# Kernel tuning notes

Measured on AMD Instinct MI355X. Metric: run time of the kernel, lower is better.

Reference implementation:

```python
import jax, jax.numpy as jnp
import numpy as np

N = 131072   # nodes
E = 2097152  # edges (avg degree 16)
B = 4096     # subgraph (center) nodes, ntype == -1
D = 64       # feature dim (in_nfeats == all latent dims)
L = 3        # number of (local, global) RelGraphConv pairs
R = 3        # num relations
NB = 2       # num bases


def setup_inputs() -> dict:
    key = jax.random.key(0)
    ks = jax.random.split(key, 20)
    s = 0.05
    return {
        "x": jax.random.normal(ks[0], (N, D), jnp.float32),
        "src": jax.random.randint(ks[1], (E,), 0, N, jnp.int32),
        "dst": jax.random.randint(ks[2], (E,), 0, N, jnp.int32),
        "etype": jax.random.randint(ks[3], (E,), 0, R, jnp.int32),
        "mask": jax.random.uniform(ks[4], (E,), jnp.float32),
        "mask2": jax.random.uniform(ks[5], (E,), jnp.float32),
        # local RelGraphConv params (basis decomposition): W_r = sum_b C[r,b] * V[b]
        "lV": jax.random.normal(ks[6], (L, NB, D, D), jnp.float32) * s,
        "lC": jax.random.normal(ks[7], (L, R, NB), jnp.float32),
        "lW": jax.random.normal(ks[8], (L, D, D), jnp.float32) * s,   # self-loop weight
        "lB": jnp.zeros((L, D), jnp.float32),
        # global RelGraphConv params
        "gV": jax.random.normal(ks[9], (L, NB, D, D), jnp.float32) * s,
        "gC": jax.random.normal(ks[10], (L, R, NB), jnp.float32),
        "gW": jax.random.normal(ks[11], (L, D, D), jnp.float32) * s,
        "gB": jnp.zeros((L, D), jnp.float32),
        # MLP head: lin1 (sum(latent_dim)=192 -> 128), lin2 (128 -> 1)
        "w1": jax.random.normal(ks[12], (128, L * D), jnp.float32) * s,
        "b1": jnp.zeros((128,), jnp.float32),
        "w2": jax.random.normal(ks[13], (1, 128), jnp.float32) * s,
        "b2": jnp.zeros((1,), jnp.float32),
        "num_subg": B,
    }


def _rel_graph_conv(h, V, C, W, b, src, dst, etype, norm):
    """Basis-decomposed RelGraphConv with self-loop (DGL semantics, eval mode)."""
    n = h.shape[0]
    hV = jnp.einsum('nd,bdo->nbo', h, V)                  # [N, NB, D]
    coef = C[etype]                                        # [E, NB] edge-type gather
    msg = jnp.einsum('eb,ebo->eo', coef, hV[src])          # [E, D]
    msg = msg * norm[:, None]                              # per-edge norm (edge_mask)
    agg = jax.ops.segment_sum(msg, dst, num_segments=n)    # scatter-add to dst
    return agg + h @ W + b                                 # + self-loop + bias


def reference(x, src, dst, etype, mask, mask2, lV, lC, lW, lB,
              gV, gC, gW, gB, w1, b1, w2, b2, num_subg):
    # eval mode: edge_drop and Dropout(0.5) are identity
    h = x
    subg_states = []
    for i in range(L):
        h = jax.nn.elu(_rel_graph_conv(h, lV[i], lC[i], lW[i], lB[i],
                                       src, dst, etype, mask))
        # (ui_states collected in original but unused for 'center' embedding)
        h = jax.nn.leaky_relu(_rel_graph_conv(h, gV[i], gC[i], gW[i], gB[i],
                                              src, dst, etype, mask2),
                              negative_slope=0.01)
        subg_states.append(h)
    subg = jnp.concatenate(subg_states, axis=1)[:num_subg]  # subgraph-center nodes
    hid = jnp.maximum(subg @ w1.T + b1, 0.0)
    out = jax.nn.sigmoid(hid @ w2.T + b2)
    return out[:, 0]
```

## Files before the change

kernel.cpp:

```cpp
#include <hip/hip_runtime.h>
#include <math.h>

#define N_NODES 131072
#define N_EDGES 2097152
#define DIM     64
#define BSUB    4096
#define NREL    3
#define NBASES  2
#define NCB     256
#define CBSZ    8192

typedef unsigned short u16;
typedef __attribute__((ext_vector_type(8))) short bf16x8;
typedef __attribute__((ext_vector_type(4))) float f32x4;

__device__ __forceinline__ float bf2f(u16 x) {
    return __uint_as_float(((unsigned)x) << 16);
}
__device__ __forceinline__ u16 f2bf(float f) {
    unsigned u = __float_as_uint(f);
    unsigned r = (u + 0x7FFFu + ((u >> 16) & 1u)) >> 16;
    return (u16)r;
}
__device__ __forceinline__ float4 bf4_to_f4(ushort4 u) {
    return make_float4(bf2f(u.x), bf2f(u.y), bf2f(u.z), bf2f(u.w));
}
__device__ __forceinline__ ushort4 f4_to_bf4(float4 v) {
    ushort4 o; o.x = f2bf(v.x); o.y = f2bf(v.y); o.z = f2bf(v.z); o.w = f2bf(v.w);
    return o;
}


__global__ void initmark_kernel(int* __restrict__ mark, int* __restrict__ chist) {
    int i = blockIdx.x * 256 + threadIdx.x;
    if (i < N_NODES) mark[i] = (i < BSUB) ? 1 : 0;
    if (i < NCB) chist[i] = 0;
}

__global__ __launch_bounds__(256) void chist_kernel(const int* __restrict__ dst,
                                                    int* __restrict__ chist) {
    __shared__ int lh[NCB];
    int tid = threadIdx.x;
    lh[tid] = 0;
    __syncthreads();
    int base = blockIdx.x * CBSZ + tid;
#pragma unroll
    for (int j = 0; j < CBSZ / 256; j++)
        atomicAdd(&lh[dst[base + j * 256] >> 9], 1);
    __syncthreads();
    atomicAdd(&chist[tid], lh[tid]);
}

__global__ void cscan_kernel(const int* __restrict__ chist, int* __restrict__ cbase,
                             int* __restrict__ ccur, int* __restrict__ offs) {
    __shared__ int s[NCB];
    int tid = threadIdx.x;
    int v = chist[tid];
    s[tid] = v;
    __syncthreads();
    int val = v;
    for (int off = 1; off < NCB; off <<= 1) {
        int tmp = (tid >= off) ? s[tid - off] : 0;
        __syncthreads();
        val += tmp;
        s[tid] = val;
        __syncthreads();
    }
    cbase[tid] = val - v;
    ccur[tid] = val - v;
    if (tid == 0) offs[N_NODES] = N_EDGES;
}

__global__ __launch_bounds__(256) void cscatter_kernel(
    const int* __restrict__ src, const int* __restrict__ dst,
    const int* __restrict__ et, const float* __restrict__ m1,
    const float* __restrict__ m2, int* __restrict__ ccur,
    int4* __restrict__ tmp, int* __restrict__ mark) {
    __shared__ int lh[NCB];
    __shared__ int lbase[NCB];
    int tid = threadIdx.x;
    lh[tid] = 0;
    __syncthreads();
    int e0 = blockIdx.x * CBSZ;
#pragma unroll
    for (int j = 0; j < CBSZ / 256; j++)
        atomicAdd(&lh[dst[e0 + tid + j * 256] >> 9], 1);
    __syncthreads();
    int c = lh[tid];
    lbase[tid] = c ? atomicAdd(&ccur[tid], c) : 0;
    lh[tid] = 0;
    __syncthreads();
#pragma unroll
    for (int j = 0; j < CBSZ / 256; j++) {
        int e = e0 + tid + j * 256;
        int d = dst[e];
        int s = src[e];
        int b = d >> 9;
        int r = atomicAdd(&lh[b], 1);
        int4 v;
        v.x = s | (et[e] << 20);
        v.y = __float_as_int(m1[e]);
        v.z = __float_as_int(m2[e]);
        v.w = d;
        tmp[lbase[b] + r] = v;
        if (d < BSUB) mark[s] = 1;
    }
}

__global__ __launch_bounds__(256) void fscatter_kernel(
    const int4* __restrict__ tmp, const int* __restrict__ cbase,
    const int* __restrict__ chist, int* __restrict__ offs,
    int4* __restrict__ csr) {
    __shared__ int lh[512];
    __shared__ int lpre[512];
    __shared__ int s2[256];
    int b = blockIdx.x;
    int tid = threadIdx.x;
    int base = cbase[b], cnt = chist[b];
    lh[tid] = 0; lh[tid + 256] = 0;
    __syncthreads();
    for (int i = tid; i < cnt; i += 256)
        atomicAdd(&lh[tmp[base + i].w & 511], 1);
    __syncthreads();
    int a0 = lh[2 * tid], a1 = lh[2 * tid + 1];
    s2[tid] = a0 + a1;
    __syncthreads();
    int val = s2[tid];
    for (int off = 1; off < 256; off <<= 1) {
        int t = (tid >= off) ? s2[tid - off] : 0;
        __syncthreads();
        val += t;
        s2[tid] = val;
        __syncthreads();
    }
    int ex = val - (a0 + a1);
    lpre[2 * tid] = ex;
    lpre[2 * tid + 1] = ex + a0;
    offs[b * 512 + 2 * tid]     = base + ex;
    offs[b * 512 + 2 * tid + 1] = base + ex + a0;
    lh[tid] = 0; lh[tid + 256] = 0;
    __syncthreads();
    for (int i = tid; i < cnt; i += 256) {
        int4 v = tmp[base + i];
        int k = v.w & 511;
        int r = atomicAdd(&lh[k], 1);
        csr[base + lpre[k] + r] = v;
    }
}

__global__ void scan1_kernel(const int* __restrict__ cnt, int* __restrict__ scanned,
                             int* __restrict__ bsum) {
    __shared__ int s[256];
    int tid = threadIdx.x;
    int i = blockIdx.x * 256 + tid;
    int v = cnt[i];
    s[tid] = v;
    __syncthreads();
    int val = v;
    for (int off = 1; off < 256; off <<= 1) {
        int tmp = (tid >= off) ? s[tid - off] : 0;
        __syncthreads();
        val += tmp;
        s[tid] = val;
        __syncthreads();
    }
    scanned[i] = val - v;
    if (tid == 255) bsum[blockIdx.x] = val;
}

__global__ void scan2_kernel(int* __restrict__ bsum) {
    __shared__ int s[512];
    int tid = threadIdx.x;
    int v = bsum[tid];
    s[tid] = v;
    __syncthreads();
    int val = v;
    for (int off = 1; off < 512; off <<= 1) {
        int tmp = (tid >= off) ? s[tid - off] : 0;
        __syncthreads();
        val += tmp;
        s[tid] = val;
        __syncthreads();
    }
    bsum[tid] = val - v;
}

__global__ void listfill_kernel(const int* __restrict__ mark, const int* __restrict__ mpref,
                                const int* __restrict__ mbsum, int* __restrict__ list,
                                int* __restrict__ nld) {
    int i = blockIdx.x * 256 + threadIdx.x;
    int pos = mpref[i] + mbsum[blockIdx.x];
    if (mark[i]) list[pos] = i;
    if (i == N_NODES - 1) *nld = pos + mark[i];
}

__global__ void cvt_kernel(const float4* __restrict__ x, ushort4* __restrict__ hb, int n4) {
    int i = blockIdx.x * 256 + threadIdx.x;
    if (i < n4) hb[i] = f4_to_bf4(x[i]);
}

__global__ void wpack_kernel(const float* __restrict__ lV, const float* __restrict__ lW,
                             const float* __restrict__ gV, const float* __restrict__ gW,
                             u16* __restrict__ wfrag) {
    int idx = blockIdx.x * 256 + threadIdx.x;
    if (idx >= 6 * 4 * 6 * 64) return;
    int lane = idx & 63;
    int kidx = (idx >> 6) % 6;
    int nt   = (idx >> 6) / 6 % 4;
    int c    = idx / (64 * 6 * 4);
    int layer = c >> 1;
    bool isglobal = c & 1;
    const float* V = isglobal ? gV : lV;
    const float* W = isglobal ? gW : lW;
    int n = nt * 16 + (lane & 15);
    int kbase = kidx * 32 + (lane >> 4) * 8;
    u16 vals[8];
#pragma unroll
    for (int j = 0; j < 8; j++) {
        int r = kbase + j;
        float val;
        if (r < NBASES * DIM) {
            int b = r >> 6, d = r & 63;
            val = V[((layer * NBASES + b) * DIM + d) * DIM + n];
        } else {
            int d = r - NBASES * DIM;
            val = W[(layer * DIM + d) * DIM + n];
        }
        vals[j] = f2bf(val);
    }
    ushort4* o = (ushort4*)(wfrag + (size_t)idx * 8);
    o[0] = make_ushort4(vals[0], vals[1], vals[2], vals[3]);
    o[1] = make_ushort4(vals[4], vals[5], vals[6], vals[7]);
}

__global__ __launch_bounds__(256) void agg_kernel(
    const ushort4* __restrict__ hb, const int* __restrict__ offs,
    const int4* __restrict__ csr, const float* __restrict__ Cc,
    int which, ushort4* __restrict__ t, int nNodes,
    const int* __restrict__ list, const int* __restrict__ nld) {
    __shared__ int4 lmeta[4][64];
    int lane = threadIdx.x & 63;
    int wid  = threadIdx.x >> 6;
    int idx = (blockIdx.x << 2) + wid;
    int n;
    if (list) {
        if (idx >= *nld) return;
        n = list[idx];
    } else {
        if (idx >= nNodes) return;
        n = idx;
    }
    int q  = lane >> 4;
    int ql = lane & 15;
    float Ca0 = Cc[0], Cb0 = Cc[1], Ca1 = Cc[2], Cb1 = Cc[3], Ca2 = Cc[4], Cb2 = Cc[5];
    int beg = offs[n], end = offs[n + 1];
    float4 a0 = make_float4(0.f, 0.f, 0.f, 0.f);
    float4 a1 = make_float4(0.f, 0.f, 0.f, 0.f);
    for (int base = beg; base < end; base += 64) {
        int cnt = min(64, end - base);
        int pp = 0; float c0 = 0.f, c1 = 0.f;
        if (lane < cnt) {
            int4 meta = csr[base + lane];
            int et = ((unsigned)meta.x) >> 20;
            float m = __int_as_float(which ? meta.z : meta.y);
            float ca = et == 0 ? Ca0 : (et == 1 ? Ca1 : Ca2);
            float cb = et == 0 ? Cb0 : (et == 1 ? Cb1 : Cb2);
            pp = (meta.x & 0xFFFFF) << 4;
            c0 = m * ca;
            c1 = m * cb;
        }
        lmeta[wid][lane] = make_int4(pp, __float_as_int(c0), __float_as_int(c1), 0);
        for (int j = 0; j < cnt; j += 16) {
#pragma unroll
            for (int s = 0; s < 4; s++) {
                int4 md = lmeta[wid][j + (s << 2) + q];
                ushort4 rv = hb[md.x + ql];
                float4 v = bf4_to_f4(rv);
                float e0 = __int_as_float(md.y);
                float e1 = __int_as_float(md.z);
                a0.x = fmaf(e0, v.x, a0.x); a0.y = fmaf(e0, v.y, a0.y);
                a0.z = fmaf(e0, v.z, a0.z); a0.w = fmaf(e0, v.w, a0.w);
                a1.x = fmaf(e1, v.x, a1.x); a1.y = fmaf(e1, v.y, a1.y);
                a1.z = fmaf(e1, v.z, a1.z); a1.w = fmaf(e1, v.w, a1.w);
            }
        }
    }
#pragma unroll
    for (int off = 16; off < 64; off <<= 1) {
        a0.x += __shfl_xor(a0.x, off, 64); a0.y += __shfl_xor(a0.y, off, 64);
        a0.z += __shfl_xor(a0.z, off, 64); a0.w += __shfl_xor(a0.w, off, 64);
        a1.x += __shfl_xor(a1.x, off, 64); a1.y += __shfl_xor(a1.y, off, 64);
        a1.z += __shfl_xor(a1.z, off, 64); a1.w += __shfl_xor(a1.w, off, 64);
    }
    ushort4 outv = f4_to_bf4(q == 0 ? a0 : a1);
    if (q < 2)
        t[(size_t)n * 32 + (q << 4) + ql] = outv;
}

__global__ __launch_bounds__(256) void gemm_kernel(
    const u16* __restrict__ t, const u16* __restrict__ h,
    const u16* __restrict__ wfrag, const float* __restrict__ bias,
    u16* __restrict__ hout, float* __restrict__ subg, int subg_off, int act,
    const int* __restrict__ list, const int* __restrict__ nld) {
    int tid = threadIdx.x;
    int wave = tid >> 6, lane = tid & 63;
    int l16 = lane & 15, quad = lane >> 4;
    int nL = list ? *nld : 0;
    if (list && blockIdx.x * 64 >= nL) return;
    int slot0 = blockIdx.x * 64 + wave * 16;
    int myslot = slot0 + l16;
    int rowA = list ? list[min(myslot, nL - 1)] : myslot;
    const u16* trow = t + (size_t)rowA * 128;
    const u16* hrow = h + (size_t)rowA * 64;
    f32x4 acc0 = {0.f, 0.f, 0.f, 0.f};
    f32x4 acc1 = {0.f, 0.f, 0.f, 0.f};
    f32x4 acc2 = {0.f, 0.f, 0.f, 0.f};
    f32x4 acc3 = {0.f, 0.f, 0.f, 0.f};
#pragma unroll
    for (int kidx = 0; kidx < 6; kidx++) {
        bf16x8 a = (kidx < 4)
            ? *(const bf16x8*)(trow + kidx * 32 + quad * 8)
            : *(const bf16x8*)(hrow + (kidx - 4) * 32 + quad * 8);
        bf16x8 b0 = *(const bf16x8*)(wfrag + ((size_t)(0 * 6 + kidx) * 64 + lane) * 8);
        bf16x8 b1 = *(const bf16x8*)(wfrag + ((size_t)(1 * 6 + kidx) * 64 + lane) * 8);
        bf16x8 b2 = *(const bf16x8*)(wfrag + ((size_t)(2 * 6 + kidx) * 64 + lane) * 8);
        bf16x8 b3 = *(const bf16x8*)(wfrag + ((size_t)(3 * 6 + kidx) * 64 + lane) * 8);
        acc0 = __builtin_amdgcn_mfma_f32_16x16x32_bf16(a, b0, acc0, 0, 0, 0);
        acc1 = __builtin_amdgcn_mfma_f32_16x16x32_bf16(a, b1, acc1, 0, 0, 0);
        acc2 = __builtin_amdgcn_mfma_f32_16x16x32_bf16(a, b2, acc2, 0, 0, 0);
        acc3 = __builtin_amdgcn_mfma_f32_16x16x32_bf16(a, b3, acc3, 0, 0, 0);
    }
    float accs[4][4] = {
        {acc0[0], acc0[1], acc0[2], acc0[3]},
        {acc1[0], acc1[1], acc1[2], acc1[3]},
        {acc2[0], acc2[1], acc2[2], acc2[3]},
        {acc3[0], acc3[1], acc3[2], acc3[3]},
    };
#pragma unroll
    for (int nt = 0; nt < 4; nt++) {
        int col = nt * 16 + l16;
        float bcol = bias[col];
#pragma unroll
        for (int r = 0; r < 4; r++) {
            int cslot = slot0 + quad * 4 + r;
            if (list && cslot >= nL) continue;
            int row = list ? __shfl(rowA, quad * 4 + r, 64) : cslot;
            float xv = accs[nt][r] + bcol;
            float v = act ? (xv > 0.f ? xv : 0.01f * xv)
                          : (xv > 0.f ? xv : expm1f(xv));
            hout[(size_t)row * 64 + col] = f2bf(v);
            if (subg && row < BSUB)
                subg[(size_t)row * 192 + subg_off + col] = v;
        }
    }
}

__global__ __launch_bounds__(256) void head_kernel(
    const float* __restrict__ subg, const float* __restrict__ w1,
    const float* __restrict__ b1, const float* __restrict__ w2,
    const float* __restrict__ b2, float* __restrict__ out) {
    __shared__ float srow[4][192];
    int lane = threadIdx.x & 63, wid = threadIdx.x >> 6;
    int row = blockIdx.x * 4 + wid;
    const float* sr = subg + (size_t)row * 192;
    srow[wid][lane] = sr[lane];
    srow[wid][64 + lane] = sr[64 + lane];
    srow[wid][128 + lane] = sr[128 + lane];
    __syncthreads();
    float acc1 = b1[lane], acc2 = b1[64 + lane];
    const float* w1a = w1 + lane * 192;
    const float* w1b = w1 + (64 + lane) * 192;
    for (int k = 0; k < 192; k++) {
        float s = srow[wid][k];
        acc1 = fmaf(s, w1a[k], acc1);
        acc2 = fmaf(s, w1b[k], acc2);
    }
    acc1 = fmaxf(acc1, 0.f);
    acc2 = fmaxf(acc2, 0.f);
    float part = acc1 * w2[lane] + acc2 * w2[64 + lane];
    for (int off = 32; off; off >>= 1) part += __shfl_down(part, off, 64);
    if (lane == 0) out[row] = 1.f / (1.f + expf(-(part + b2[0])));
}

extern "C" void kernel_launch(void* const* d_in, const int* in_sizes, int n_in,
                              void* d_out, int out_size, void* d_ws, size_t ws_size,
                              hipStream_t stream) {
    const float* x     = (const float*)d_in[0];
    const int*   src   = (const int*)d_in[1];
    const int*   dst   = (const int*)d_in[2];
    const int*   etype = (const int*)d_in[3];
    const float* mask  = (const float*)d_in[4];
    const float* mask2 = (const float*)d_in[5];
    const float* lV = (const float*)d_in[6];
    const float* lC = (const float*)d_in[7];
    const float* lW = (const float*)d_in[8];
    const float* lB = (const float*)d_in[9];
    const float* gV = (const float*)d_in[10];
    const float* gC = (const float*)d_in[11];
    const float* gW = (const float*)d_in[12];
    const float* gB = (const float*)d_in[13];
    const float* w1 = (const float*)d_in[14];
    const float* b1 = (const float*)d_in[15];
    const float* w2 = (const float*)d_in[16];
    const float* b2 = (const float*)d_in[17];
    float* out = (float*)d_out;

    char* ws = (char*)d_ws;
    size_t off = 0;
    auto alloc = [&](size_t bytes) {
        void* p = ws + off;
        off += (bytes + 255) & ~(size_t)255;
        return p;
    };
    ushort4* h    = (ushort4*)alloc((size_t)N_NODES * 64 * 2);
    ushort4* t    = (ushort4*)alloc((size_t)N_NODES * 128 * 2);
    int4*  csr    = (int4*)alloc((size_t)N_EDGES * 16);
    int*   offs   = (int*)alloc((size_t)(N_NODES + 1) * 4);
    int*   chist  = (int*)alloc(NCB * 4);
    int*   cbase  = (int*)alloc(NCB * 4);
    int*   ccur   = (int*)alloc(NCB * 4);
    int*   bsum   = (int*)alloc(512 * 4);
    int*   mark   = (int*)alloc((size_t)N_NODES * 4);
    int*   mpref  = (int*)alloc((size_t)N_NODES * 4);
    int*   mbsum  = (int*)alloc(512 * 4);
    int*   list   = (int*)alloc((size_t)N_NODES * 4);
    int*   nld    = (int*)alloc(256);
    u16*   wfrag  = (u16*)alloc((size_t)6 * 4 * 6 * 64 * 8 * 2);
    float* subg   = (float*)alloc((size_t)BSUB * 192 * 4);
    int4*  tmp    = (int4*)t;

    initmark_kernel<<<N_NODES / 256, 256, 0, stream>>>(mark, chist);
    chist_kernel<<<NCB, 256, 0, stream>>>(dst, chist);
    cscan_kernel<<<1, NCB, 0, stream>>>(chist, cbase, ccur, offs);
    cscatter_kernel<<<NCB, 256, 0, stream>>>(src, dst, etype, mask, mask2,
                                             ccur, tmp, mark);
    fscatter_kernel<<<NCB, 256, 0, stream>>>(tmp, cbase, chist, offs, csr);
    scan1_kernel<<<N_NODES / 256, 256, 0, stream>>>(mark, mpref, mbsum);
    scan2_kernel<<<1, 512, 0, stream>>>(mbsum);
    listfill_kernel<<<N_NODES / 256, 256, 0, stream>>>(mark, mpref, mbsum, list, nld);
    wpack_kernel<<<(6 * 4 * 6 * 64 + 255) / 256, 256, 0, stream>>>(lV, lW, gV, gW, wfrag);
    cvt_kernel<<<(N_NODES * 64 / 4) / 256, 256, 0, stream>>>((const float4*)x, h,
                                                             N_NODES * 64 / 4);

    const int convfrag = 4 * 6 * 64 * 8;
    for (int layer = 0; layer < 3; layer++) {
        const int* ll  = (layer == 2) ? list : nullptr;
        agg_kernel<<<N_NODES / 4, 256, 0, stream>>>(h, offs, csr,
            lC + layer * NREL * NBASES, 0, t, N_NODES, ll, nld);
        gemm_kernel<<<N_NODES / 64, 256, 0, stream>>>(
            (const u16*)t, (const u16*)h,
            wfrag + (size_t)(layer * 2 + 0) * convfrag, lB + layer * 64,
            (u16*)h, nullptr, 0, 0, ll, nld);
        int nG = (layer == 2) ? BSUB : N_NODES;
        agg_kernel<<<(nG + 3) / 4, 256, 0, stream>>>(h, offs, csr,
            gC + layer * NREL * NBASES, 1, t, nG, nullptr, nld);
        gemm_kernel<<<nG / 64, 256, 0, stream>>>(
            (const u16*)t, (const u16*)h,
            wfrag + (size_t)(layer * 2 + 1) * convfrag, gB + layer * 64,
            (u16*)h, subg, layer * 64, 1, nullptr, nld);
    }
    head_kernel<<<BSUB / 4, 256, 0, stream>>>(subg, w1, b1, w2, b2, out);
}
```

Before: 622.2 us.

## Use 512 coarse buckets and vectorize edge loads in CSR build kernels

The coarse dst bucketing for the CSR build goes from 256 buckets of 512 nodes to 512 buckets of 256 nodes. The fine scatter therefore runs 512 blocks, each with 256-entry histograms and a single-element-per-thread scan. The histogram, coarse scatter and fine scatter kernels now read edges as int4 vectors, with four items per thread. The goal is more parallelism and fewer load instructions in the preprocessing phase, at the cost of more global atomics on the coarse cursor and a launch geometry that depends on exact divisibility and alignment.

Result: faster. 603.3 us (-3.0%).

```diff
diff --git a/kernel.cpp b/kernel.cpp
--- a/kernel.cpp
+++ b/kernel.cpp
@@ -7,7 +7,7 @@
 #define BSUB    4096
 #define NREL    3
 #define NBASES  2
-#define NCB     256
+#define NCB     512
 #define CBSZ    8192
 
 typedef unsigned short u16;
@@ -41,14 +41,20 @@
                                                     int* __restrict__ chist) {
     __shared__ int lh[NCB];
     int tid = threadIdx.x;
-    lh[tid] = 0;
-    __syncthreads();
-    int base = blockIdx.x * CBSZ + tid;
-#pragma unroll
-    for (int j = 0; j < CBSZ / 256; j++)
-        atomicAdd(&lh[dst[base + j * 256] >> 9], 1);
+    lh[tid] = 0; lh[tid + 256] = 0;
+    __syncthreads();
+    int base = blockIdx.x * CBSZ;
+#pragma unroll
+    for (int j = 0; j < CBSZ / 1024; j++) {
+        int4 d4 = *(const int4*)(dst + base + j * 1024 + tid * 4);
+        atomicAdd(&lh[d4.x >> 8], 1);
+        atomicAdd(&lh[d4.y >> 8], 1);
+        atomicAdd(&lh[d4.z >> 8], 1);
+        atomicAdd(&lh[d4.w >> 8], 1);
+    }
     __syncthreads();
     atomicAdd(&chist[tid], lh[tid]);
+    atomicAdd(&chist[tid + 256], lh[tid + 256]);
 }
 
 __global__ void cscan_kernel(const int* __restrict__ chist, int* __restrict__ cbase,
@@ -71,7 +77,7 @@
     if (tid == 0) offs[N_NODES] = N_EDGES;
 }
 
-__global__ __launch_bounds__(256) void cscatter_kernel(
+__global__ __launch_bounds__(512) void cscatter_kernel(
     const int* __restrict__ src, const int* __restrict__ dst,
     const int* __restrict__ et, const float* __restrict__ m1,
     const float* __restrict__ m2, int* __restrict__ ccur,
@@ -81,29 +87,42 @@
     int tid = threadIdx.x;
     lh[tid] = 0;
     __syncthreads();
-    int e0 = blockIdx.x * CBSZ;
-#pragma unroll
-    for (int j = 0; j < CBSZ / 256; j++)
-        atomicAdd(&lh[dst[e0 + tid + j * 256] >> 9], 1);
+    int e0b = blockIdx.x * CBSZ;
+#pragma unroll
+    for (int j = 0; j < CBSZ / 2048; j++) {
+        int4 d4 = *(const int4*)(dst + e0b + j * 2048 + tid * 4);
+        atomicAdd(&lh[d4.x >> 8], 1);
+        atomicAdd(&lh[d4.y >> 8], 1);
+        atomicAdd(&lh[d4.z >> 8], 1);
+        atomicAdd(&lh[d4.w >> 8], 1);
+    }
     __syncthreads();
     int c = lh[tid];
     lbase[tid] = c ? atomicAdd(&ccur[tid], c) : 0;
     lh[tid] = 0;
     __syncthreads();
 #pragma unroll
-    for (int j = 0; j < CBSZ / 256; j++) {
-        int e = e0 + tid + j * 256;
-        int d = dst[e];
-        int s = src[e];
-        int b = d >> 9;
-        int r = atomicAdd(&lh[b], 1);
-        int4 v;
-        v.x = s | (et[e] << 20);
-        v.y = __float_as_int(m1[e]);
-        v.z = __float_as_int(m2[e]);
-        v.w = d;
-        tmp[lbase[b] + r] = v;
-        if (d < BSUB) mark[s] = 1;
+    for (int j = 0; j < CBSZ / 2048; j++) {
+        int e0 = e0b + j * 2048 + tid * 4;
+        int4  d4 = *(const int4*)(dst + e0);
+        int4  s4 = *(const int4*)(src + e0);
+        int4  t4 = *(const int4*)(et + e0);
+        float4 a4 = *(const float4*)(m1 + e0);
+        float4 b4 = *(const float4*)(m2 + e0);
+#pragma unroll
+        for (int k = 0; k < 4; k++) {
+            int d = (&d4.x)[k];
+            int s = (&s4.x)[k];
+            int b = d >> 8;
+            int r = atomicAdd(&lh[b], 1);
+            int4 v;
+            v.x = s | ((&t4.x)[k] << 20);
+            v.y = __float_as_int((&a4.x)[k]);
+            v.z = __float_as_int((&b4.x)[k]);
+            v.w = d;
+            tmp[lbase[b] + r] = v;
+            if (d < BSUB) mark[s] = 1;
+        }
     }
 }
 
@@ -111,40 +130,60 @@
     const int4* __restrict__ tmp, const int* __restrict__ cbase,
     const int* __restrict__ chist, int* __restrict__ offs,
     int4* __restrict__ csr) {
-    __shared__ int lh[512];
-    __shared__ int lpre[512];
-    __shared__ int s2[256];
+    __shared__ int lh[256];
+    __shared__ int lpre[256];
+    __shared__ int s[256];
     int b = blockIdx.x;
     int tid = threadIdx.x;
     int base = cbase[b], cnt = chist[b];
-    lh[tid] = 0; lh[tid + 256] = 0;
-    __syncthreads();
-    for (int i = tid; i < cnt; i += 256)
-        atomicAdd(&lh[tmp[base + i].w & 511], 1);
-    __syncthreads();
-    int a0 = lh[2 * tid], a1 = lh[2 * tid + 1];
-    s2[tid] = a0 + a1;
-    __syncthreads();
-    int val = s2[tid];
+    lh[tid] = 0;
+    __syncthreads();
+    int i = 0;
+    for (; i + 1024 <= cnt; i += 1024) {
+        int4 v0 = tmp[base + i + tid * 4 + 0];
+        int4 v1 = tmp[base + i + tid * 4 + 1];
+        int4 v2 = tmp[base + i + tid * 4 + 2];
+        int4 v3 = tmp[base + i + tid * 4 + 3];
+        atomicAdd(&lh[v0.w & 255], 1);
+        atomicAdd(&lh[v1.w & 255], 1);
+        atomicAdd(&lh[v2.w & 255], 1);
+        atomicAdd(&lh[v3.w & 255], 1);
+    }
+    for (int k = i + tid; k < cnt; k += 256)
+        atomicAdd(&lh[tmp[base + k].w & 255], 1);
+    __syncthreads();
+    int v = lh[tid];
+    s[tid] = v;
+    __syncthreads();
+    int val = v;
     for (int off = 1; off < 256; off <<= 1) {
-        int t = (tid >= off) ? s2[tid - off] : 0;
-        __syncthreads();
-        val += t;
-        s2[tid] = val;
-        __syncthreads();
-    }
-    int ex = val - (a0 + a1);
-    lpre[2 * tid] = ex;
-    lpre[2 * tid + 1] = ex + a0;
-    offs[b * 512 + 2 * tid]     = base + ex;
-    offs[b * 512 + 2 * tid + 1] = base + ex + a0;
-    lh[tid] = 0; lh[tid + 256] = 0;
-    __syncthreads();
-    for (int i = tid; i < cnt; i += 256) {
-        int4 v = tmp[base + i];
-        int k = v.w & 511;
+        int tq = (tid >= off) ? s[tid - off] : 0;
+        __syncthreads();
+        val += tq;
+        s[tid] = val;
+        __syncthreads();
+    }
+    int ex = val - v;
+    lpre[tid] = ex;
+    offs[b * 256 + tid] = base + ex;
+    lh[tid] = 0;
+    __syncthreads();
+    i = 0;
+    for (; i + 1024 <= cnt; i += 1024) {
+        int4 v0 = tmp[base + i + tid * 4 + 0];
+        int4 v1 = tmp[base + i + tid * 4 + 1];
+        int4 v2 = tmp[base + i + tid * 4 + 2];
+        int4 v3 = tmp[base + i + tid * 4 + 3];
+        int k0 = v0.w & 255; int r0 = atomicAdd(&lh[k0], 1); csr[base + lpre[k0] + r0] = v0;
+        int k1 = v1.w & 255; int r1 = atomicAdd(&lh[k1], 1); csr[base + lpre[k1] + r1] = v1;
+        int k2 = v2.w & 255; int r2 = atomicAdd(&lh[k2], 1); csr[base + lpre[k2] + r2] = v2;
+        int k3 = v3.w & 255; int r3 = atomicAdd(&lh[k3], 1); csr[base + lpre[k3] + r3] = v3;
+    }
+    for (int kk = i + tid; kk < cnt; kk += 256) {
+        int4 vv = tmp[base + kk];
+        int k = vv.w & 255;
         int r = atomicAdd(&lh[k], 1);
-        csr[base + lpre[k] + r] = v;
+        csr[base + lpre[k] + r] = vv;
     }
 }
 
@@ -430,10 +469,10 @@
     int4*  tmp    = (int4*)t;
 
     initmark_kernel<<<N_NODES / 256, 256, 0, stream>>>(mark, chist);
-    chist_kernel<<<NCB, 256, 0, stream>>>(dst, chist);
+    chist_kernel<<<N_EDGES / CBSZ, 256, 0, stream>>>(dst, chist);
     cscan_kernel<<<1, NCB, 0, stream>>>(chist, cbase, ccur, offs);
-    cscatter_kernel<<<NCB, 256, 0, stream>>>(src, dst, etype, mask, mask2,
-                                             ccur, tmp, mark);
+    cscatter_kernel<<<N_EDGES / CBSZ, 512, 0, stream>>>(src, dst, etype, mask, mask2,
+                                                        ccur, tmp, mark);
     fscatter_kernel<<<NCB, 256, 0, stream>>>(tmp, cbase, chist, offs, csr);
     scan1_kernel<<<N_NODES / 256, 256, 0, stream>>>(mark, mpref, mbsum);
     scan2_kernel<<<1, 512, 0, stream>>>(mbsum);
```
